# Optimization experiments

Hardware: AMD Instinct MI355X
Metric: run time of the kernel (lower is better)

The kernel has to match this reference:

```python
import jax, jax.numpy as jnp
import numpy as np

B, T, DIM = 4, 2048, 512
HEADS, HD = 8, 64
RANK = 256
WIN = 256
EPS = 1e-6
ROPE_BASE = 10000.0


def _rope_tables(seq_len, head_dim):
    pos = jnp.arange(seq_len, dtype=jnp.float32)                      # [T]
    inv_freq = 1.0 / (ROPE_BASE ** (jnp.arange(0, head_dim, 2, dtype=jnp.float32) / head_dim))  # [HD/2]
    ang = pos[:, None] * inv_freq[None, :]                            # [T, HD/2]
    cos = jnp.concatenate([jnp.cos(ang), jnp.cos(ang)], axis=-1)      # [T, HD]
    sin = jnp.concatenate([jnp.sin(ang), jnp.sin(ang)], axis=-1)
    return cos, sin


def _rotate_half(x):
    x1, x2 = jnp.split(x, 2, axis=-1)
    return jnp.concatenate([-x2, x1], axis=-1)


def _apply_rope(q, k):
    # q, k: [B, H, T, HD]
    cos, sin = _rope_tables(q.shape[2], q.shape[3])
    cos = cos[None, None]; sin = sin[None, None]
    q = q * cos + _rotate_half(q) * sin
    k = k * cos + _rotate_half(k) * sin
    return q, k


def _rmsnorm(x, w):
    x32 = x.astype(jnp.float32)
    n = x32 * jax.lax.rsqrt(jnp.mean(x32 * x32, axis=-1, keepdims=True) + EPS)
    return n.astype(x.dtype) * w


def setup_inputs() -> dict:
    key = jax.random.key(0)
    ks = jax.random.split(key, 6)
    s = 0.02
    return {
        "x": jax.random.normal(ks[0], (B, T, DIM), dtype=jnp.float32),
        "Wq": jax.random.normal(ks[1], (DIM, DIM), dtype=jnp.float32) * s,
        "Wkv_down": jax.random.normal(ks[2], (RANK, DIM), dtype=jnp.float32) * s,
        "kv_norm_w": jnp.ones((RANK,), dtype=jnp.float32),
        "Wkv_up": jax.random.normal(ks[3], (2 * DIM, RANK), dtype=jnp.float32) * s,
        "Wout": jax.random.normal(ks[4], (DIM, DIM), dtype=jnp.float32) * s,
    }


def reference(x, Wq, Wkv_down, kv_norm_w, Wkv_up, Wout):
    # q projection -> [B, H, T, HD]
    q = jnp.einsum('btd,ed->bte', x, Wq).reshape(B, T, HEADS, HD).transpose(0, 2, 1, 3)
    # latent KV: down-proj -> RMSNorm -> up-proj
    c_kv = jnp.einsum('btd,rd->btr', x, Wkv_down)          # [B, T, RANK]
    c_kv = _rmsnorm(c_kv, kv_norm_w)
    kv = jnp.einsum('btr,er->bte', c_kv, Wkv_up)            # [B, T, 2*DIM]
    kv = kv.reshape(B, T, 2, HEADS, HD).transpose(2, 0, 3, 1, 4)
    k, v = kv[0], kv[1]                                     # [B, H, T, HD]
    q, k = _apply_rope(q, k)
    rows = jnp.arange(T)[:, None]
    cols = jnp.arange(T)[None, :]
    mask = jnp.abs(cols - rows) <= WIN                      # [T, T]
    scale = HD ** -0.5
    scores = jnp.einsum('bhtd,bhsd->bhts', q, k) * scale    # [B, H, T, T]
    scores = jnp.where(mask[None, None], scores, jnp.float32(-jnp.inf))
    attn = jax.nn.softmax(scores, axis=-1)
    out = jnp.einsum('bhts,bhsd->bhtd', attn, v)            # [B, H, T, HD]
    out = out.transpose(0, 2, 1, 3).reshape(B, T, DIM)
    return jnp.einsum('btd,ed->bte', out, Wout)
```

## Files before the change

### kernel.cpp

```cpp
#include <hip/hip_runtime.h>
#include <math.h>

#define BB 4
#define TT 2048
#define DIMM 512
#define HEADS 8
#define HDIM 64
#define RANKK 256
#define WINN 256

static constexpr int BT = BB * TT;
#define SC2 0.1803368801111244f

typedef short bf8_t __attribute__((ext_vector_type(8)));
typedef float f32x4 __attribute__((ext_vector_type(4)));

__device__ __forceinline__ unsigned f2bf2(float a, float b) {
    unsigned r;
    asm("v_cvt_pk_bf16_f32 %0, %1, %2" : "=v"(r) : "v"(a), "v"(b));
    return r;
}

typedef __attribute__((address_space(1))) void gvoid_t;
typedef __attribute__((address_space(3))) void lvoid_t;
__device__ __forceinline__ void gload16(const void* g, void* l) {
    __builtin_amdgcn_global_load_lds((gvoid_t*)g, (lvoid_t*)l, 16, 0, 0);
}
#define WAIT_VM0_BARRIER() do { \
    asm volatile("s_waitcnt vmcnt(0)" ::: "memory"); \
    __builtin_amdgcn_s_barrier(); \
    __builtin_amdgcn_sched_barrier(0); \
} while (0)

__device__ __forceinline__ void cvt4(const float* __restrict__ s,
                                     unsigned short* __restrict__ d, int i) {
    float4 v = *reinterpret_cast<const float4*>(s + i);
    uint2 st = make_uint2(f2bf2(v.x, v.y), f2bf2(v.z, v.w));
    *reinterpret_cast<uint2*>(d + i) = st;
}

__global__ __launch_bounds__(256) void prep_kernel(
    const float* __restrict__ x, const float* __restrict__ Wq,
    const float* __restrict__ Wkd, const float* __restrict__ Wku,
    const float* __restrict__ wn, const float* __restrict__ Wout,
    unsigned short* __restrict__ xb, unsigned short* __restrict__ wcomb,
    unsigned short* __restrict__ wkub, unsigned short* __restrict__ woutb,
    float* __restrict__ cosT, float* __restrict__ sinT) {
    int bid = blockIdx.x;
    if (bid < 4096) {
        cvt4(x, xb, (bid * 256 + threadIdx.x) * 4);
    } else if (bid < 4352) {
        cvt4(Wq, wcomb, ((bid - 4096) * 256 + threadIdx.x) * 4);
    } else if (bid < 4480) {
        cvt4(Wkd, wcomb + DIMM * DIMM, ((bid - 4352) * 256 + threadIdx.x) * 4);
    } else if (bid < 4736) {
        int i = ((bid - 4480) * 256 + threadIdx.x) * 4;
        float4 v = *reinterpret_cast<const float4*>(Wku + i);
        float4 s = *reinterpret_cast<const float4*>(wn + (i & 255));
        uint2 st = make_uint2(f2bf2(v.x * s.x, v.y * s.y), f2bf2(v.z * s.z, v.w * s.w));
        *reinterpret_cast<uint2*>(wkub + i) = st;
    } else if (bid < 4992) {
        cvt4(Wout, woutb, ((bid - 4736) * 256 + threadIdx.x) * 4);
    } else {
        int idx = (bid - 4992) * 256 + threadIdx.x;
        int t = idx >> 5, f = idx & 31;
        double frev = exp2(-(double)f * 0.4152410118609203) * 0.15915494309189535;
        double a = (double)t * frev;
        float fr = (float)(a - floor(a));
        cosT[idx] = cospif(2.0f * fr);
        sinT[idx] = sinpif(2.0f * fr);
    }
}

template<int MODE, int BM>
__global__ __launch_bounds__(BM * 4) void gemm_bf(const unsigned short* __restrict__ A,
                                                  const unsigned short* __restrict__ W,
                                                  float* __restrict__ Cf,
                                                  unsigned short* __restrict__ O1,
                                                  unsigned short* __restrict__ O2,
                                                  const float* __restrict__ cosT,
                                                  const float* __restrict__ sinT,
                                                  float* __restrict__ ssum,
                                                  int K, int N) {
    __shared__ __align__(16) unsigned short As[2][BM * 64];
    __shared__ __align__(16) unsigned short Ws[2][128 * 64];
    const int tid = threadIdx.x;
    const int lane = tid & 63, w = tid >> 6;
    const int lr = lane & 15, hi = lane >> 4;
    const int m0 = blockIdx.x * BM, n0 = blockIdx.y * 128;
    const int wr = (w >> 1) * 32, wc = (w & 1) * 64;

    f32x4 acc[2][4];
#pragma unroll
    for (int i = 0; i < 2; ++i)
#pragma unroll
        for (int j = 0; j < 4; ++j) acc[i][j] = 0.0f;

    const int NT = K >> 6;
    auto stage = [&](int t, int b) {
        const int kt = t * 64;
#pragma unroll
        for (int c = tid; c < BM * 8; c += BM * 4) {
            int row = c >> 3, sc = ((c & 7) ^ (row & 7)) << 3;
            gload16(A + (size_t)(m0 + row) * K + kt + sc, &As[b][c * 8]);
        }
#pragma unroll
        for (int c = tid; c < 1024; c += BM * 4) {
            int row = c >> 3, sc = ((c & 7) ^ (row & 7)) << 3;
            gload16(W + (size_t)(n0 + row) * K + kt + sc, &Ws[b][c * 8]);
        }
    };

    stage(0, 0);
    WAIT_VM0_BARRIER();
    for (int t = 0; t < NT; ++t) {
        const int cur = t & 1;
        if (t + 1 < NT) stage(t + 1, cur ^ 1);
        bf8_t af[2][2], bw[4][2];
#pragma unroll
        for (int i = 0; i < 2; ++i) {
            int row = wr + i * 16 + lr;
#pragma unroll
            for (int kk = 0; kk < 2; ++kk)
                af[i][kk] = *reinterpret_cast<const bf8_t*>(
                    &As[cur][row * 64 + (((kk * 4 + hi) ^ (row & 7)) << 3)]);
        }
#pragma unroll
        for (int j = 0; j < 4; ++j) {
            int row = wc + j * 16 + lr;
#pragma unroll
            for (int kk = 0; kk < 2; ++kk)
                bw[j][kk] = *reinterpret_cast<const bf8_t*>(
                    &Ws[cur][row * 64 + (((kk * 4 + hi) ^ (row & 7)) << 3)]);
        }
#pragma unroll
        for (int kk = 0; kk < 2; ++kk)
#pragma unroll
            for (int i = 0; i < 2; ++i)
#pragma unroll
                for (int j = 0; j < 4; ++j)
                    acc[i][j] = __builtin_amdgcn_mfma_f32_16x16x32_bf16(af[i][kk], bw[j][kk], acc[i][j], 0, 0, 0);
        if (t + 1 < NT) WAIT_VM0_BARRIER();
    }

    if constexpr (MODE == 0) {
#pragma unroll
        for (int i = 0; i < 2; ++i)
#pragma unroll
            for (int j = 0; j < 4; ++j)
#pragma unroll
                for (int r = 0; r < 4; ++r)
                    Cf[(size_t)(m0 + wr + i * 16 + 4 * hi + r) * N + n0 + wc + j * 16 + lr] = acc[i][j][r];
    } else if (n0 < 512) {
        int h = (n0 + wc) >> 6;
#pragma unroll
        for (int i = 0; i < 2; ++i) {
            int tb = m0 + wr + i * 16 + 4 * hi;
            float4 rv4 = make_float4(1.f, 1.f, 1.f, 1.f);
            if constexpr (MODE == 2) {
                float4 sa = *reinterpret_cast<const float4*>(ssum + tb);
                float4 sb = *reinterpret_cast<const float4*>(ssum + 8192 + tb);
                float4 sc = *reinterpret_cast<const float4*>(ssum + 16384 + tb);
                float4 sd = *reinterpret_cast<const float4*>(ssum + 24576 + tb);
                rv4.x = rsqrtf((sa.x + sb.x + sc.x + sd.x) * (1.0f / RANKK) + 1e-6f);
                rv4.y = rsqrtf((sa.y + sb.y + sc.y + sd.y) * (1.0f / RANKK) + 1e-6f);
                rv4.z = rsqrtf((sa.z + sb.z + sc.z + sd.z) * (1.0f / RANKK) + 1e-6f);
                rv4.w = rsqrtf((sa.w + sb.w + sc.w + sd.w) * (1.0f / RANKK) + 1e-6f);
            }
#pragma unroll
            for (int j = 0; j < 2; ++j)
#pragma unroll
                for (int r = 0; r < 4; ++r) {
                    int t = tb + r;
                    int b = t >> 11, tt = t & 2047;
                    int ff = j * 16 + lr;
                    float rv = (&rv4.x)[r];
                    float x1 = acc[i][j][r] * rv, x2 = acc[i][j + 2][r] * rv;
                    float cc = cosT[tt * 32 + ff], ss = sinT[tt * 32 + ff];
                    unsigned u = f2bf2(x1 * cc - x2 * ss, x2 * cc + x1 * ss);
                    unsigned short* dp = O1 + ((size_t)((b * 8 + h) * 2048 + tt)) * 64;
                    dp[ff]      = (unsigned short)u;
                    dp[ff + 32] = (unsigned short)(u >> 16);
                }
        }
    } else if constexpr (MODE == 1) {
        int cb = n0 - 512 + wc;
        int part = ((n0 - 512) >> 7) * 2 + (w & 1);
#pragma unroll
        for (int i = 0; i < 2; ++i) {
            int tb = m0 + wr + i * 16 + 4 * hi;
#pragma unroll
            for (int r = 0; r < 4; ++r) {
                float ps = acc[i][0][r] * acc[i][0][r] + acc[i][1][r] * acc[i][1][r]
                         + acc[i][2][r] * acc[i][2][r] + acc[i][3][r] * acc[i][3][r];
                ps += __shfl_xor(ps, 1);
                ps += __shfl_xor(ps, 2);
                ps += __shfl_xor(ps, 4);
                ps += __shfl_xor(ps, 8);
                if (lr == 0) ssum[part * 8192 + tb + r] = ps;
            }
#pragma unroll
            for (int j = 0; j < 4; ++j) {
                unsigned a01 = f2bf2(acc[i][j][0], acc[i][j][1]);
                unsigned a23 = f2bf2(acc[i][j][2], acc[i][j][3]);
                unsigned short* dp = O2 + (size_t)tb * 256 + cb + j * 16 + lr;
                dp[0]   = (unsigned short)a01;
                dp[256] = (unsigned short)(a01 >> 16);
                dp[512] = (unsigned short)a23;
                dp[768] = (unsigned short)(a23 >> 16);
            }
        }
    } else {
        int cb = n0 + wc - 512;
        int h = cb >> 6;
#pragma unroll
        for (int i = 0; i < 2; ++i) {
            int tb = m0 + wr + i * 16 + 4 * hi;
            int b = tb >> 11, tt = tb & 2047;
            float4 sa = *reinterpret_cast<const float4*>(ssum + tb);
            float4 sb = *reinterpret_cast<const float4*>(ssum + 8192 + tb);
            float4 sc = *reinterpret_cast<const float4*>(ssum + 16384 + tb);
            float4 sd = *reinterpret_cast<const float4*>(ssum + 24576 + tb);
            float4 rv4;
            rv4.x = rsqrtf((sa.x + sb.x + sc.x + sd.x) * (1.0f / RANKK) + 1e-6f);
            rv4.y = rsqrtf((sa.y + sb.y + sc.y + sd.y) * (1.0f / RANKK) + 1e-6f);
            rv4.z = rsqrtf((sa.z + sb.z + sc.z + sd.z) * (1.0f / RANKK) + 1e-6f);
            rv4.w = rsqrtf((sa.w + sb.w + sc.w + sd.w) * (1.0f / RANKK) + 1e-6f);
#pragma unroll
            for (int j = 0; j < 4; ++j) {
                int hd = j * 16 + lr;
                uint2 st = make_uint2(f2bf2(acc[i][j][0] * rv4.x, acc[i][j][1] * rv4.y),
                                      f2bf2(acc[i][j][2] * rv4.z, acc[i][j][3] * rv4.w));
                *reinterpret_cast<uint2*>(O2 + (((size_t)(b * 8 + h) * 64 + hd) * 2048 + tt)) = st;
            }
        }
    }
}

__global__ __launch_bounds__(512) void attn_mfma(const unsigned short* __restrict__ qbf,
                                                 const unsigned short* __restrict__ kbf,
                                                 const unsigned short* __restrict__ vT,
                                                 unsigned short* __restrict__ aob) {
    __shared__ __align__(16) unsigned short Kl[2][64 * 64];
    __shared__ __align__(16) unsigned short Vl[2][64 * 64];
    __shared__ unsigned short Pl[128][72];
    const int tid = threadIdx.x;
    const int lane = tid & 63, w = tid >> 6;
    const int lr = lane & 15, hi = lane >> 4;

    const int fid = blockIdx.x;
    const int swz = (fid & 7) * 64 + (fid >> 3);
    const int t0 = (swz & 15) * 128;
    const int bh = swz >> 4;

    const unsigned short* qp = qbf + ((size_t)bh * TT + t0 + w * 16 + lr) * HDIM;
    bf8_t qa[2];
    qa[0] = *reinterpret_cast<const bf8_t*>(qp + hi * 8);
    qa[1] = *reinterpret_cast<const bf8_t*>(qp + 32 + hi * 8);

    f32x4 oc[4];
#pragma unroll
    for (int f = 0; f < 4; ++f) oc[f] = 0.0f;
    float lp[4] = {0.f, 0.f, 0.f, 0.f};

    const int smin = max(0, t0 - WINN);
    const int smax = min(TT, t0 + 128 + WINN);
    const int NT = (smax - smin) >> 6;

    const int st_row = tid >> 3;
    const int st_c = tid & 7;
    const int st_cs = (st_c ^ (st_row & 7)) << 3;

    auto stage = [&](int t, int b) {
        const int s0 = smin + t * 64;
        gload16(kbf + ((size_t)bh * TT + s0 + st_row) * HDIM + st_cs, &Kl[b][tid * 8]);
        gload16(vT + ((size_t)bh * 64 + st_row) * TT + s0 + st_cs, &Vl[b][tid * 8]);
    };

    stage(0, 0);
    WAIT_VM0_BARRIER();
    for (int t = 0; t < NT; ++t) {
        const int cur = t & 1;
        if (t + 1 < NT) stage(t + 1, cur ^ 1);
        const int s0 = smin + t * 64;
        const int off_w = s0 - t0 - w * 16;
        const bool active = (off_w >= -(WINN + 63)) && (off_w <= WINN + 15);

        if (active) {
            f32x4 sacc[4];
#pragma unroll
            for (int f = 0; f < 4; ++f) sacc[f] = 0.0f;
            __builtin_amdgcn_s_setprio(1);
#pragma unroll
            for (int ks = 0; ks < 2; ++ks)
#pragma unroll
                for (int f = 0; f < 4; ++f) {
                    int row = f * 16 + lr;
                    bf8_t kb = *reinterpret_cast<const bf8_t*>(
                        &Kl[cur][row * 64 + (((ks * 4 + hi) ^ (row & 7)) << 3)]);
                    sacc[f] = __builtin_amdgcn_mfma_f32_16x16x32_bf16(qa[ks], kb, sacc[f], 0, 0, 0);
                }
            __builtin_amdgcn_s_setprio(0);

            const bool edge = (off_w + 63 > WINN) || (off_w - 15 < -WINN);
#pragma unroll
            for (int f = 0; f < 4; ++f) {
                float p[4];
#pragma unroll
                for (int r = 0; r < 4; ++r) {
                    float v;
                    if (edge) {
                        int d = off_w + f * 16 + lr - 4 * hi - r;
                        v = (d <= WINN && d >= -WINN) ? exp2f(sacc[f][r] * SC2) : 0.f;
                    } else {
                        v = exp2f(sacc[f][r] * SC2);
                    }
                    p[r] = v;
                    lp[r] += v;
                }
                unsigned a01 = f2bf2(p[0], p[1]);
                unsigned a23 = f2bf2(p[2], p[3]);
                unsigned short* bp = &Pl[w * 16 + 4 * hi][f * 16 + lr];
                bp[0]   = (unsigned short)a01;
                bp[72]  = (unsigned short)(a01 >> 16);
                bp[144] = (unsigned short)a23;
                bp[216] = (unsigned short)(a23 >> 16);
            }

            __builtin_amdgcn_s_setprio(1);
#pragma unroll
            for (int ks = 0; ks < 2; ++ks) {
                bf8_t pa = *reinterpret_cast<const bf8_t*>(&Pl[w * 16 + lr][ks * 32 + hi * 8]);
#pragma unroll
                for (int f = 0; f < 4; ++f) {
                    int row = f * 16 + lr;
                    bf8_t vb = *reinterpret_cast<const bf8_t*>(
                        &Vl[cur][row * 64 + (((ks * 4 + hi) ^ (row & 7)) << 3)]);
                    oc[f] = __builtin_amdgcn_mfma_f32_16x16x32_bf16(pa, vb, oc[f], 0, 0, 0);
                }
            }
            __builtin_amdgcn_s_setprio(0);
        }
        if (t + 1 < NT) WAIT_VM0_BARRIER();
    }

#pragma unroll
    for (int r = 0; r < 4; ++r) {
        lp[r] += __shfl_xor(lp[r], 1);
        lp[r] += __shfl_xor(lp[r], 2);
        lp[r] += __shfl_xor(lp[r], 4);
        lp[r] += __shfl_xor(lp[r], 8);
    }

    int b = bh >> 3, h = bh & 7;
#pragma unroll
    for (int r = 0; r < 4; ++r) {
        float inv = 1.0f / lp[r];
        int t = t0 + w * 16 + 4 * hi + r;
        unsigned short* op = aob + ((size_t)b * TT + t) * DIMM + h * HDIM;
        unsigned u0 = f2bf2(oc[0][r] * inv, oc[1][r] * inv);
        unsigned u1 = f2bf2(oc[2][r] * inv, oc[3][r] * inv);
        op[lr]      = (unsigned short)u0;
        op[16 + lr] = (unsigned short)(u0 >> 16);
        op[32 + lr] = (unsigned short)u1;
        op[48 + lr] = (unsigned short)(u1 >> 16);
    }
}

extern "C" void kernel_launch(void* const* d_in, const int* in_sizes, int n_in,
                              void* d_out, int out_size, void* d_ws, size_t ws_size,
                              hipStream_t stream) {
    const float* x     = (const float*)d_in[0];
    const float* Wq    = (const float*)d_in[1];
    const float* Wkd   = (const float*)d_in[2];
    const float* wnorm = (const float*)d_in[3];
    const float* Wku   = (const float*)d_in[4];
    const float* Wout  = (const float*)d_in[5];
    float* out = (float*)d_out;
    char* ws = (char*)d_ws;

    unsigned short* xb    = (unsigned short*)(ws + 0);
    unsigned short* qb    = (unsigned short*)(ws + 8388608);
    unsigned short* kb    = (unsigned short*)(ws + 16777216);
    unsigned short* vTb   = (unsigned short*)(ws + 25165824);
    unsigned short* ckvb0 = (unsigned short*)(ws + 33554432);
    unsigned short* aob   = (unsigned short*)(ws + 37748736);
    unsigned short* wcomb = (unsigned short*)(ws + 46137344);
    unsigned short* wkub  = (unsigned short*)(ws + 46923776);
    unsigned short* woutb = (unsigned short*)(ws + 47448064);
    float*          cosT  = (float*)(ws + 48005120);
    float*          sinT  = (float*)(ws + 48267264);
    float*          ssum  = (float*)(ws + 48529408);

    prep_kernel<<<5248, 256, 0, stream>>>(x, Wq, Wkd, Wku, wnorm, Wout,
                                          xb, wcomb, wkub, woutb, cosT, sinT);

    gemm_bf<1, 128><<<dim3(BT / 128, 6), 512, 0, stream>>>(xb, wcomb, nullptr, qb, ckvb0,
                                                           cosT, sinT, ssum, DIMM, 768);

    gemm_bf<2, 128><<<dim3(BT / 128, 8), 512, 0, stream>>>(ckvb0, wkub, nullptr, kb, vTb,
                                                           cosT, sinT, ssum, RANKK, 1024);

    attn_mfma<<<512, 512, 0, stream>>>(qb, kb, vTb, aob);

    gemm_bf<0, 64><<<dim3(BT / 64, 4), 256, 0, stream>>>(aob, woutb, out, nullptr, nullptr,
                                                         nullptr, nullptr, nullptr, DIMM, DIMM);
}
```

Baseline: 72.01 us.

## Fuse fp32-to-bf16 conversion of x into the QKV-down GEMM A-tile staging

Removes the separate x conversion pass from the prep kernel and instead has the first GEMM load fp32 x tiles into registers, convert to bf16 and write swizzled into shared memory after the MFMAs of the current tile. This eliminates a full write and reread of the bf16 copy of x and shrinks the prep launch. In exchange, each GEMM block reads twice the bytes for A, repeated across the six N-blocks, and the barrier now also waits on LDS counters.

```diff
diff --git a/kernel.cpp b/kernel.cpp
--- a/kernel.cpp
+++ b/kernel.cpp
@@ -27,7 +27,7 @@
     __builtin_amdgcn_global_load_lds((gvoid_t*)g, (lvoid_t*)l, 16, 0, 0);
 }
 #define WAIT_VM0_BARRIER() do { \
-    asm volatile("s_waitcnt vmcnt(0)" ::: "memory"); \
+    asm volatile("s_waitcnt vmcnt(0) lgkmcnt(0)" ::: "memory"); \
     __builtin_amdgcn_s_barrier(); \
     __builtin_amdgcn_sched_barrier(0); \
 } while (0)
@@ -40,29 +40,27 @@
 }
 
 __global__ __launch_bounds__(256) void prep_kernel(
-    const float* __restrict__ x, const float* __restrict__ Wq,
-    const float* __restrict__ Wkd, const float* __restrict__ Wku,
-    const float* __restrict__ wn, const float* __restrict__ Wout,
-    unsigned short* __restrict__ xb, unsigned short* __restrict__ wcomb,
-    unsigned short* __restrict__ wkub, unsigned short* __restrict__ woutb,
+    const float* __restrict__ Wq, const float* __restrict__ Wkd,
+    const float* __restrict__ Wku, const float* __restrict__ wn,
+    const float* __restrict__ Wout,
+    unsigned short* __restrict__ wcomb, unsigned short* __restrict__ wkub,
+    unsigned short* __restrict__ woutb,
     float* __restrict__ cosT, float* __restrict__ sinT) {
     int bid = blockIdx.x;
-    if (bid < 4096) {
-        cvt4(x, xb, (bid * 256 + threadIdx.x) * 4);
-    } else if (bid < 4352) {
-        cvt4(Wq, wcomb, ((bid - 4096) * 256 + threadIdx.x) * 4);
-    } else if (bid < 4480) {
-        cvt4(Wkd, wcomb + DIMM * DIMM, ((bid - 4352) * 256 + threadIdx.x) * 4);
-    } else if (bid < 4736) {
-        int i = ((bid - 4480) * 256 + threadIdx.x) * 4;
+    if (bid < 256) {
+        cvt4(Wq, wcomb, (bid * 256 + threadIdx.x) * 4);
+    } else if (bid < 384) {
+        cvt4(Wkd, wcomb + DIMM * DIMM, ((bid - 256) * 256 + threadIdx.x) * 4);
+    } else if (bid < 640) {
+        int i = ((bid - 384) * 256 + threadIdx.x) * 4;
         float4 v = *reinterpret_cast<const float4*>(Wku + i);
         float4 s = *reinterpret_cast<const float4*>(wn + (i & 255));
         uint2 st = make_uint2(f2bf2(v.x * s.x, v.y * s.y), f2bf2(v.z * s.z, v.w * s.w));
         *reinterpret_cast<uint2*>(wkub + i) = st;
-    } else if (bid < 4992) {
-        cvt4(Wout, woutb, ((bid - 4736) * 256 + threadIdx.x) * 4);
+    } else if (bid < 896) {
+        cvt4(Wout, woutb, ((bid - 640) * 256 + threadIdx.x) * 4);
     } else {
-        int idx = (bid - 4992) * 256 + threadIdx.x;
+        int idx = (bid - 896) * 256 + threadIdx.x;
         int t = idx >> 5, f = idx & 31;
         double frev = exp2(-(double)f * 0.4152410118609203) * 0.15915494309189535;
         double a = (double)t * frev;
@@ -90,6 +88,12 @@
     const int m0 = blockIdx.x * BM, n0 = blockIdx.y * 128;
     const int wr = (w >> 1) * 32, wc = (w & 1) * 64;
 
+    const float* A32 = (const float*)A;
+    float4 pnd[4];
+    const int arow = tid >> 2;
+    const int ac0 = (tid & 3) * 16;
+    const int wch0 = (tid & 3) * 2;
+
     f32x4 acc[2][4];
 #pragma unroll
     for (int i = 0; i < 2; ++i)
@@ -97,12 +101,33 @@
         for (int j = 0; j < 4; ++j) acc[i][j] = 0.0f;
 
     const int NT = K >> 6;
-    auto stage = [&](int t, int b) {
+    auto stageA = [&](int t) {
+        if constexpr (MODE == 1) {
+            const float* ap = A32 + (size_t)(m0 + arow) * K + t * 64 + ac0;
+            pnd[0] = *reinterpret_cast<const float4*>(ap);
+            pnd[1] = *reinterpret_cast<const float4*>(ap + 4);
+            pnd[2] = *reinterpret_cast<const float4*>(ap + 8);
+            pnd[3] = *reinterpret_cast<const float4*>(ap + 12);
+        }
+    };
+    auto stageAw = [&](int b) {
+        unsigned u0 = f2bf2(pnd[0].x, pnd[0].y), u1 = f2bf2(pnd[0].z, pnd[0].w);
+        unsigned u2 = f2bf2(pnd[1].x, pnd[1].y), u3 = f2bf2(pnd[1].z, pnd[1].w);
+        unsigned u4 = f2bf2(pnd[2].x, pnd[2].y), u5 = f2bf2(pnd[2].z, pnd[2].w);
+        unsigned u6 = f2bf2(pnd[3].x, pnd[3].y), u7 = f2bf2(pnd[3].z, pnd[3].w);
+        *reinterpret_cast<uint4*>(&As[b][arow * 64 + ((wch0 ^ (arow & 7)) << 3)]) =
+            make_uint4(u0, u1, u2, u3);
+        *reinterpret_cast<uint4*>(&As[b][arow * 64 + (((wch0 + 1) ^ (arow & 7)) << 3)]) =
+            make_uint4(u4, u5, u6, u7);
+    };
+    auto stageG = [&](int t, int b) {
         const int kt = t * 64;
-#pragma unroll
-        for (int c = tid; c < BM * 8; c += BM * 4) {
-            int row = c >> 3, sc = ((c & 7) ^ (row & 7)) << 3;
-            gload16(A + (size_t)(m0 + row) * K + kt + sc, &As[b][c * 8]);
+        if constexpr (MODE != 1) {
+#pragma unroll
+            for (int c = tid; c < BM * 8; c += BM * 4) {
+                int row = c >> 3, sc = ((c & 7) ^ (row & 7)) << 3;
+                gload16(A + (size_t)(m0 + row) * K + kt + sc, &As[b][c * 8]);
+            }
         }
 #pragma unroll
         for (int c = tid; c < 1024; c += BM * 4) {
@@ -111,11 +136,13 @@
         }
     };
 
-    stage(0, 0);
+    stageA(0);
+    stageG(0, 0);
+    if constexpr (MODE == 1) stageAw(0);
     WAIT_VM0_BARRIER();
     for (int t = 0; t < NT; ++t) {
         const int cur = t & 1;
-        if (t + 1 < NT) stage(t + 1, cur ^ 1);
+        if (t + 1 < NT) { stageA(t + 1); stageG(t + 1, cur ^ 1); }
         bf8_t af[2][2], bw[4][2];
 #pragma unroll
         for (int i = 0; i < 2; ++i) {
@@ -140,7 +167,10 @@
 #pragma unroll
                 for (int j = 0; j < 4; ++j)
                     acc[i][j] = __builtin_amdgcn_mfma_f32_16x16x32_bf16(af[i][kk], bw[j][kk], acc[i][j], 0, 0, 0);
-        if (t + 1 < NT) WAIT_VM0_BARRIER();
+        if (t + 1 < NT) {
+            if constexpr (MODE == 1) stageAw(cur ^ 1);
+            WAIT_VM0_BARRIER();
+        }
     }
 
     if constexpr (MODE == 0) {
@@ -379,7 +409,6 @@
     float* out = (float*)d_out;
     char* ws = (char*)d_ws;
 
-    unsigned short* xb    = (unsigned short*)(ws + 0);
     unsigned short* qb    = (unsigned short*)(ws + 8388608);
     unsigned short* kb    = (unsigned short*)(ws + 16777216);
     unsigned short* vTb   = (unsigned short*)(ws + 25165824);
@@ -392,10 +421,11 @@
     float*          sinT  = (float*)(ws + 48267264);
     float*          ssum  = (float*)(ws + 48529408);
 
-    prep_kernel<<<5248, 256, 0, stream>>>(x, Wq, Wkd, Wku, wnorm, Wout,
-                                          xb, wcomb, wkub, woutb, cosT, sinT);
-
-    gemm_bf<1, 128><<<dim3(BT / 128, 6), 512, 0, stream>>>(xb, wcomb, nullptr, qb, ckvb0,
+    prep_kernel<<<1152, 256, 0, stream>>>(Wq, Wkd, Wku, wnorm, Wout,
+                                          wcomb, wkub, woutb, cosT, sinT);
+
+    gemm_bf<1, 128><<<dim3(BT / 128, 6), 512, 0, stream>>>((const unsigned short*)x, wcomb,
+                                                           nullptr, qb, ckvb0,
                                                            cosT, sinT, ssum, DIMM, 768);
 
     gemm_bf<2, 128><<<dim3(BT / 128, 8), 512, 0, stream>>>(ckvb0, wkub, nullptr, kb, vTb,
```

Result: slower. 74.07 us (+2.9%).
